# Performance work log

Measured on AMD Instinct MI355X. Metric: run time of the kernel, lower is better.

The kernel has to match this reference:

```python
import jax, jax.numpy as jnp
import numpy as np

N_NODES = 20000
N_EDGES = 640000
FEAT = 128


def setup_inputs() -> dict:
    key = jax.random.key(0)
    k1, k2, k3, k4 = jax.random.split(key, 4)
    x = jax.random.normal(k1, (1, N_NODES, FEAT, 4), dtype=jnp.float32)
    edge_index = jax.random.randint(k2, (2, N_EDGES), 0, N_NODES, dtype=jnp.int64)
    # Linear(in_channels=128, out_channels=128): W [out, in], b [out]
    W = jax.random.normal(k3, (FEAT, FEAT), dtype=jnp.float32) * 0.05
    b = jax.random.normal(k4, (FEAT,), dtype=jnp.float32) * 0.05
    return {"x": x, "edge_index": edge_index, "W": W, "b": b}


def reference(x, edge_index, W, b):
    # x: [B, N, F, T]
    B, N, F, T = x.shape
    # permute -> [B, T, N, F]; Linear over feature dim (out == in == F)
    h = jnp.einsum('bnft,of->btno', x, W) + b          # [B, T, N, F]
    h = h.reshape(B * T, N, F)                          # flatten batch*time
    src = edge_index[0]  # message source (x_j)
    dst = edge_index[1]  # scatter target
    msgs = h[:, src, :]                                 # [B*T, E, F] gather
    # scatter-max per target node (PyG aggr='max'); vmap over batch*time
    agg = jax.vmap(lambda m: jax.ops.segment_max(m, dst, num_segments=N))(msgs)
    # nodes with no incoming edges: segment_max yields -inf -> 0 (PyG fill)
    agg = jnp.where(jnp.isneginf(agg), jnp.zeros_like(agg), agg)
    out = agg.reshape(B, T, N, F).transpose(0, 2, 3, 1)  # [B, N, F, T]
    return out
```

## Files before the change

kernel.cpp:

```cpp
#include <hip/hip_runtime.h>
#include <hip/hip_bf16.h>
#include <stdint.h>

#define N_NODES 20000
#define N_EDGES 640000
#define FEAT 128
#define CAPD 128
#define NPHASE 8
#define CNTSTRIDE 16

typedef __attribute__((ext_vector_type(8))) short bf16x8;
typedef __attribute__((ext_vector_type(4))) float f32x4;

__device__ __forceinline__ unsigned pkbf16(float lo, float hi) {
  __hip_bfloat162 p = __float22bfloat162_rn(make_float2(lo, hi));
  return *reinterpret_cast<unsigned*>(&p);
}

__device__ __forceinline__ unsigned short enc16(float f) {
  unsigned a = __float_as_uint(f);
  unsigned b = (a + 0x7FFFu + ((a >> 16) & 1u)) >> 16;
  unsigned s = (unsigned)((int)a >> 31);
  return (unsigned short)((b ^ 0x8000u) ^ (s & 0x7FFFu));
}

__device__ __forceinline__ float dec16(unsigned e) {
  unsigned b = (e & 0x8000u) ? (e ^ 0x8000u) : (e ^ 0xFFFFu);
  return __uint_as_float(b << 16);
}

__device__ __forceinline__ void pmax(unsigned& a, unsigned v) {
  asm("v_pk_max_u16 %0, %0, %1" : "+v"(a) : "v"(v));
}

#define PMX4(v)                                              \
  do {                                                       \
    pmax(a0, (v).x); pmax(a1, (v).y);                        \
    pmax(a2, (v).z); pmax(a3, (v).w);                        \
  } while (0)

__global__ void init_kernel(const float* __restrict__ W,
                            unsigned short* __restrict__ Wbf,
                            int* __restrict__ cnt) {
  int i = blockIdx.x * 256 + threadIdx.x;
  if (i < N_NODES * CNTSTRIDE) cnt[i] = 0;
  if (i < FEAT * FEAT / 2) {
    float2 w = ((const float2*)W)[i];
    ((unsigned*)Wbf)[i] = pkbf16(w.x, w.y);
  }
}

__global__ __launch_bounds__(256) void gemm_scatter_kernel(
    const float4* __restrict__ x, const unsigned short* __restrict__ Wbf,
    const float* __restrict__ b, uint4* __restrict__ h,
    const int* __restrict__ ei, int* __restrict__ cnt,
    unsigned short* __restrict__ csr) {
  __shared__ __align__(16) unsigned short sm[17408 / 2];
  const int tid = threadIdx.x;
  const int n0 = blockIdx.x * 16;

#pragma unroll
  for (int r = 0; r < 2; ++r) {
    int e = blockIdx.x * 512 + r * 256 + tid;
    int src = ei[e];
    int dst = ei[N_EDGES + e];
    int pos = atomicAdd(&cnt[dst * CNTSTRIDE], 1);
    if (pos < CAPD) csr[(size_t)dst * CAPD + pos] = (unsigned short)src;
  }

#pragma unroll
  for (int it = 0; it < 4; ++it) {
    int e = tid + it * 256;
    int n = e >> 6, fp = e & 63;
    float4 a = x[(size_t)(n0 + n) * 128 + 2 * fp];
    float4 c = x[(size_t)(n0 + n) * 128 + 2 * fp + 1];
    ((unsigned*)sm)[(0 * 16 + n) * 68 + fp] = pkbf16(a.x, c.x);
    ((unsigned*)sm)[(1 * 16 + n) * 68 + fp] = pkbf16(a.y, c.y);
    ((unsigned*)sm)[(2 * 16 + n) * 68 + fp] = pkbf16(a.z, c.z);
    ((unsigned*)sm)[(3 * 16 + n) * 68 + fp] = pkbf16(a.w, c.w);
  }

  __syncthreads();

  const int wv = tid >> 6;
  const int l = tid & 63;
  const int col = l & 15;
  const int quad = l >> 4;

  f32x4 acc[8];
#pragma unroll
  for (int os = 0; os < 8; ++os) {
    float bv = b[os * 16 + col];
    acc[os] = (f32x4){bv, bv, bv, bv};
  }

#pragma unroll
  for (int k = 0; k < 4; ++k) {
    bf16x8 af = *(const bf16x8*)&sm[(wv * 16 + col) * 136 + k * 32 + quad * 8];
#pragma unroll
    for (int os = 0; os < 8; ++os) {
      bf16x8 bfv = *(const bf16x8*)&Wbf[(os * 16 + col) * 128 + k * 32 + quad * 8];
      acc[os] = __builtin_amdgcn_mfma_f32_16x16x32_bf16(af, bfv, acc[os], 0, 0, 0);
    }
  }

  __syncthreads();

#pragma unroll
  for (int os = 0; os < 8; ++os) {
#pragma unroll
    for (int r = 0; r < 4; ++r) {
      sm[(quad * 4 + r) * 520 + (os * 16 + col) * 4 + wv] = enc16(acc[os][r]);
    }
  }
  __syncthreads();

#pragma unroll
  for (int it = 0; it < 4; ++it) {
    int e = tid + it * 256;
    int n = e >> 6, q = e & 63;
    uint4 v = *(const uint4*)&sm[n * 520 + q * 8];
    h[(size_t)(n0 + n) * 64 + q] = v;
  }
}

#define CLAMP8(P, ivv, base)                                            \
  int P##0 = ((base) + 0 < deg) ? (int)((ivv).x & 0xFFFFu) : idx0;      \
  int P##1 = ((base) + 1 < deg) ? (int)((ivv).x >> 16) : idx0;          \
  int P##2 = ((base) + 2 < deg) ? (int)((ivv).y & 0xFFFFu) : idx0;      \
  int P##3 = ((base) + 3 < deg) ? (int)((ivv).y >> 16) : idx0;          \
  int P##4 = ((base) + 4 < deg) ? (int)((ivv).z & 0xFFFFu) : idx0;      \
  int P##5 = ((base) + 5 < deg) ? (int)((ivv).z >> 16) : idx0;          \
  int P##6 = ((base) + 6 < deg) ? (int)((ivv).w & 0xFFFFu) : idx0;      \
  int P##7 = ((base) + 7 < deg) ? (int)((ivv).w >> 16) : idx0;

#define ISSUE8(V, P)                                                    \
  V##0 = *(const uint4*)(hb + (((unsigned)P##0 << 10) + pb));           \
  V##1 = *(const uint4*)(hb + (((unsigned)P##1 << 10) + pb));           \
  V##2 = *(const uint4*)(hb + (((unsigned)P##2 << 10) + pb));           \
  V##3 = *(const uint4*)(hb + (((unsigned)P##3 << 10) + pb));           \
  V##4 = *(const uint4*)(hb + (((unsigned)P##4 << 10) + pb));           \
  V##5 = *(const uint4*)(hb + (((unsigned)P##5 << 10) + pb));           \
  V##6 = *(const uint4*)(hb + (((unsigned)P##6 << 10) + pb));           \
  V##7 = *(const uint4*)(hb + (((unsigned)P##7 << 10) + pb));

#define PMAX8(V)                                                        \
  do {                                                                  \
    PMX4(V##0); PMX4(V##1); PMX4(V##2); PMX4(V##3);                     \
    PMX4(V##4); PMX4(V##5); PMX4(V##6); PMX4(V##7);                     \
  } while (0)

__global__ __launch_bounds__(256, 4) void agg_kernel(
    const uint4* __restrict__ h, const int* __restrict__ cnt,
    const unsigned short* __restrict__ csr, float4* __restrict__ out) {
  __shared__ __align__(16) unsigned short sidx[32][136];
  const int bid = blockIdx.x;
  const int p = bid & 7;
  const int grp = bid >> 3;
  const int n0 = grp * 32;
  const int tid = threadIdx.x;

  {
    int r = tid >> 3;
    int q = tid & 7;
    const uint4* srow = (const uint4*)(csr + (size_t)(n0 + r) * CAPD);
    *(uint4*)&sidx[r][q * 8] = srow[q];
    *(uint4*)&sidx[r][(q + 8) * 8] = srow[q + 8];
  }
  __syncthreads();

  const int w = tid >> 6;
  const int lane = tid & 63;
  const int g = lane >> 3;
  const int oq = lane & 7;
  const int n = n0 + w * 8 + g;

  int deg = cnt[n * CNTSTRIDE];
  deg = deg > CAPD ? CAPD : deg;

  const unsigned short* myrow = sidx[w * 8 + g];
  int idx0 = (deg > 0) ? (int)myrow[0] : 0;

  int dmax = deg;
#pragma unroll
  for (int d = 8; d <= 32; d <<= 1) {
    int o = __shfl_xor(dmax, d);
    dmax = o > dmax ? o : dmax;
  }
  dmax = __builtin_amdgcn_readfirstlane(dmax);

  unsigned a0 = 0x007F007Fu, a1 = a0, a2 = a0, a3 = a0;
  const char* hb = (const char*)h;
  const unsigned pb = (((unsigned)p * 8 + oq) << 4);

  if (dmax > 0) {
    const int dmax16 = (dmax + 15) & ~15;
    uint4 vA0, vA1, vA2, vA3, vA4, vA5, vA6, vA7;
    uint4 vB0, vB1, vB2, vB3, vB4, vB5, vB6, vB7;
    {
      uint4 iv = *(const uint4*)&myrow[0];
      CLAMP8(eA, iv, 0);
      ISSUE8(vA, eA);
    }
    int jb = 0;
    while (true) {
      {
        uint4 iv = *(const uint4*)&myrow[jb + 8];
        CLAMP8(eB, iv, jb + 8);
        ISSUE8(vB, eB);
      }
      PMAX8(vA);
      jb += 16;
      if (jb >= dmax16) {
        PMAX8(vB);
        break;
      }
      {
        uint4 iv = *(const uint4*)&myrow[jb];
        CLAMP8(eA2, iv, jb);
        ISSUE8(vA, eA2);
      }
      PMAX8(vB);
    }
  }

  float4 o0, o1;
  if (deg == 0) {
    o0 = make_float4(0.f, 0.f, 0.f, 0.f);
    o1 = o0;
  } else {
    o0 = make_float4(dec16(a0 & 0xFFFFu), dec16(a0 >> 16),
                     dec16(a1 & 0xFFFFu), dec16(a1 >> 16));
    o1 = make_float4(dec16(a2 & 0xFFFFu), dec16(a2 >> 16),
                     dec16(a3 & 0xFFFFu), dec16(a3 >> 16));
  }
  out[(size_t)n * 128 + p * 16 + oq * 2] = o0;
  out[(size_t)n * 128 + p * 16 + oq * 2 + 1] = o1;
}

extern "C" void kernel_launch(void* const* d_in, const int* in_sizes, int n_in,
                              void* d_out, int out_size, void* d_ws, size_t ws_size,
                              hipStream_t stream) {
  const float* x = (const float*)d_in[0];
  const int* ei = (const int*)d_in[1];
  const float* W = (const float*)d_in[2];
  const float* b = (const float*)d_in[3];
  float* out = (float*)d_out;

  char* ws = (char*)d_ws;
  uint4* h = (uint4*)ws;
  int* cnt = (int*)(ws + 20480000);
  unsigned short* csr = (unsigned short*)(ws + 21760000);
  unsigned short* Wbf = (unsigned short*)(ws + 26880000);

  init_kernel<<<(N_NODES * CNTSTRIDE + 255) / 256, 256, 0, stream>>>(W, Wbf, cnt);
  gemm_scatter_kernel<<<N_NODES / 16, 256, 0, stream>>>((const float4*)x, Wbf, b, h,
                                                        ei, cnt, csr);
  agg_kernel<<<(N_NODES / 32) * NPHASE, 256, 0, stream>>>(h, cnt, csr, (float4*)out);
}
```

Before: 195.8 us.

## Split scatter and GEMM into specialized blocks, stage W in LDS, drop init kernel

The init kernel is replaced by a memset, and W is now converted to bf16 into LDS inside each GEMM block. The GEMM/scatter kernel now uses 512-thread blocks, with every third block doing only edge scatter and the other two each computing a 16-node tile, 8 waves splitting the output columns. This is meant to cut a launch, put the atomic scatter and the MFMA work in separate blocks so they overlap, and read W from LDS instead of global. In exchange, every GEMM block redundantly converts the full W matrix, and the agg kernel loses its occupancy hint.

```diff
diff --git a/kernel.cpp b/kernel.cpp
--- a/kernel.cpp
+++ b/kernel.cpp
@@ -39,46 +39,64 @@
     pmax(a2, (v).z); pmax(a3, (v).w);                        \
   } while (0)
 
-__global__ void init_kernel(const float* __restrict__ W,
-                            unsigned short* __restrict__ Wbf,
-                            int* __restrict__ cnt) {
-  int i = blockIdx.x * 256 + threadIdx.x;
-  if (i < N_NODES * CNTSTRIDE) cnt[i] = 0;
-  if (i < FEAT * FEAT / 2) {
-    float2 w = ((const float2*)W)[i];
-    ((unsigned*)Wbf)[i] = pkbf16(w.x, w.y);
-  }
-}
-
-__global__ __launch_bounds__(256) void gemm_scatter_kernel(
-    const float4* __restrict__ x, const unsigned short* __restrict__ Wbf,
+__global__ __launch_bounds__(512) void gemm_scatter_kernel(
+    const float4* __restrict__ x, const float* __restrict__ W,
     const float* __restrict__ b, uint4* __restrict__ h,
     const int* __restrict__ ei, int* __restrict__ cnt,
     unsigned short* __restrict__ csr) {
   __shared__ __align__(16) unsigned short sm[17408 / 2];
+  __shared__ __align__(16) unsigned short Wlds[128 * 136];
   const int tid = threadIdx.x;
-  const int n0 = blockIdx.x * 16;
-
-#pragma unroll
-  for (int r = 0; r < 2; ++r) {
-    int e = blockIdx.x * 512 + r * 256 + tid;
-    int src = ei[e];
-    int dst = ei[N_EDGES + e];
-    int pos = atomicAdd(&cnt[dst * CNTSTRIDE], 1);
-    if (pos < CAPD) csr[(size_t)dst * CAPD + pos] = (unsigned short)src;
-  }
-
-#pragma unroll
-  for (int it = 0; it < 4; ++it) {
-    int e = tid + it * 256;
-    int n = e >> 6, fp = e & 63;
-    float4 a = x[(size_t)(n0 + n) * 128 + 2 * fp];
-    float4 c = x[(size_t)(n0 + n) * 128 + 2 * fp + 1];
-    ((unsigned*)sm)[(0 * 16 + n) * 68 + fp] = pkbf16(a.x, c.x);
-    ((unsigned*)sm)[(1 * 16 + n) * 68 + fp] = pkbf16(a.y, c.y);
-    ((unsigned*)sm)[(2 * 16 + n) * 68 + fp] = pkbf16(a.z, c.z);
-    ((unsigned*)sm)[(3 * 16 + n) * 68 + fp] = pkbf16(a.w, c.w);
-  }
+  const int bid = blockIdx.x;
+  const int m3 = bid % 3;
+
+  if (m3 == 2) {
+    const int base = (bid / 3) * 1024;
+#pragma unroll
+    for (int r = 0; r < 2; ++r) {
+      int e = base + r * 512 + tid;
+      int src = ei[e];
+      int dst = ei[N_EDGES + e];
+      int pos = atomicAdd(&cnt[dst * CNTSTRIDE], 1);
+      if (pos < CAPD) csr[(size_t)dst * CAPD + pos] = (unsigned short)src;
+    }
+    return;
+  }
+
+  const int tile = (bid / 3) * 2 + m3;
+  const int n0 = tile * 16;
+
+  {
+    const float4* Wv = (const float4*)W;
+    const int o = tid >> 2;
+    const int q0 = (tid & 3) * 8;
+    float4 wa[8];
+#pragma unroll
+    for (int q = 0; q < 8; ++q) wa[q] = Wv[o * 32 + q0 + q];
+    unsigned* wrow = (unsigned*)&Wlds[o * 136] + (tid & 3) * 16;
+#pragma unroll
+    for (int q = 0; q < 8; ++q) {
+      wrow[2 * q] = pkbf16(wa[q].x, wa[q].y);
+      wrow[2 * q + 1] = pkbf16(wa[q].z, wa[q].w);
+    }
+  }
+
+  const int e0 = tid, e1 = tid + 512;
+  const int na = e0 >> 6, fa = e0 & 63;
+  const int nb = e1 >> 6, fb = e1 & 63;
+  float4 a0 = x[(size_t)(n0 + na) * 128 + 2 * fa];
+  float4 c0 = x[(size_t)(n0 + na) * 128 + 2 * fa + 1];
+  float4 a1 = x[(size_t)(n0 + nb) * 128 + 2 * fb];
+  float4 c1 = x[(size_t)(n0 + nb) * 128 + 2 * fb + 1];
+
+  ((unsigned*)sm)[(0 * 16 + na) * 68 + fa] = pkbf16(a0.x, c0.x);
+  ((unsigned*)sm)[(1 * 16 + na) * 68 + fa] = pkbf16(a0.y, c0.y);
+  ((unsigned*)sm)[(2 * 16 + na) * 68 + fa] = pkbf16(a0.z, c0.z);
+  ((unsigned*)sm)[(3 * 16 + na) * 68 + fa] = pkbf16(a0.w, c0.w);
+  ((unsigned*)sm)[(0 * 16 + nb) * 68 + fb] = pkbf16(a1.x, c1.x);
+  ((unsigned*)sm)[(1 * 16 + nb) * 68 + fb] = pkbf16(a1.y, c1.y);
+  ((unsigned*)sm)[(2 * 16 + nb) * 68 + fb] = pkbf16(a1.z, c1.z);
+  ((unsigned*)sm)[(3 * 16 + nb) * 68 + fb] = pkbf16(a1.w, c1.w);
 
   __syncthreads();
 
@@ -86,20 +104,23 @@
   const int l = tid & 63;
   const int col = l & 15;
   const int quad = l >> 4;
-
-  f32x4 acc[8];
-#pragma unroll
-  for (int os = 0; os < 8; ++os) {
-    float bv = b[os * 16 + col];
+  const int t = wv & 3;
+  const int osh = wv >> 2;
+
+  f32x4 acc[4];
+#pragma unroll
+  for (int os = 0; os < 4; ++os) {
+    float bv = b[(osh * 4 + os) * 16 + col];
     acc[os] = (f32x4){bv, bv, bv, bv};
   }
 
 #pragma unroll
   for (int k = 0; k < 4; ++k) {
-    bf16x8 af = *(const bf16x8*)&sm[(wv * 16 + col) * 136 + k * 32 + quad * 8];
-#pragma unroll
-    for (int os = 0; os < 8; ++os) {
-      bf16x8 bfv = *(const bf16x8*)&Wbf[(os * 16 + col) * 128 + k * 32 + quad * 8];
+    bf16x8 af = *(const bf16x8*)&sm[(t * 16 + col) * 136 + k * 32 + quad * 8];
+#pragma unroll
+    for (int os = 0; os < 4; ++os) {
+      bf16x8 bfv =
+          *(const bf16x8*)&Wlds[((osh * 4 + os) * 16 + col) * 136 + k * 32 + quad * 8];
       acc[os] = __builtin_amdgcn_mfma_f32_16x16x32_bf16(af, bfv, acc[os], 0, 0, 0);
     }
   }
@@ -107,17 +128,17 @@
   __syncthreads();
 
 #pragma unroll
-  for (int os = 0; os < 8; ++os) {
+  for (int os = 0; os < 4; ++os) {
 #pragma unroll
     for (int r = 0; r < 4; ++r) {
-      sm[(quad * 4 + r) * 520 + (os * 16 + col) * 4 + wv] = enc16(acc[os][r]);
-    }
-  }
-  __syncthreads();
-
-#pragma unroll
-  for (int it = 0; it < 4; ++it) {
-    int e = tid + it * 256;
+      sm[(quad * 4 + r) * 520 + ((osh * 4 + os) * 16 + col) * 4 + t] = enc16(acc[os][r]);
+    }
+  }
+  __syncthreads();
+
+#pragma unroll
+  for (int it = 0; it < 2; ++it) {
+    int e = tid + it * 512;
     int n = e >> 6, q = e & 63;
     uint4 v = *(const uint4*)&sm[n * 520 + q * 8];
     h[(size_t)(n0 + n) * 64 + q] = v;
@@ -150,7 +171,7 @@
     PMX4(V##4); PMX4(V##5); PMX4(V##6); PMX4(V##7);                     \
   } while (0)
 
-__global__ __launch_bounds__(256, 4) void agg_kernel(
+__global__ __launch_bounds__(256) void agg_kernel(
     const uint4* __restrict__ h, const int* __restrict__ cnt,
     const unsigned short* __restrict__ csr, float4* __restrict__ out) {
   __shared__ __align__(16) unsigned short sidx[32][136];
@@ -251,10 +272,9 @@
   uint4* h = (uint4*)ws;
   int* cnt = (int*)(ws + 20480000);
   unsigned short* csr = (unsigned short*)(ws + 21760000);
-  unsigned short* Wbf = (unsigned short*)(ws + 26880000);
-
-  init_kernel<<<(N_NODES * CNTSTRIDE + 255) / 256, 256, 0, stream>>>(W, Wbf, cnt);
-  gemm_scatter_kernel<<<N_NODES / 16, 256, 0, stream>>>((const float4*)x, Wbf, b, h,
-                                                        ei, cnt, csr);
+
+  hipMemsetAsync(cnt, 0, N_NODES * CNTSTRIDE * sizeof(int), stream);
+  gemm_scatter_kernel<<<1875, 512, 0, stream>>>((const float4*)x, W, b, h,
+                                                ei, cnt, csr);
   agg_kernel<<<(N_NODES / 32) * NPHASE, 256, 0, stream>>>(h, cnt, csr, (float4*)out);
 }
```

Measured after the change: 164.2 us. -16.1%, faster.
